# Kernel optimization log

Hardware: AMD Instinct MI355X
Metric: run time of the kernel (lower is better)

The kernel has to match this reference:

```python
import jax, jax.numpy as jnp
import numpy as np

H = 16      # num_heads
D = 64      # head_dim
SCALE = (2 * D) ** -0.5


def setup_inputs() -> dict:
    key = jax.random.key(0)
    k1, k2, k3, k4, k5 = jax.random.split(key, 5)
    tokens = jax.random.normal(k1, (4, 2048, 1024), dtype=jnp.float32)
    sen = jax.random.normal(k2, (4, 1, 1024), dtype=jnp.float32)
    W1 = jax.random.normal(k3, (1024, 3072), dtype=jnp.float32) * (1024 ** -0.5)
    W2 = jax.random.normal(k4, (1024, 2048), dtype=jnp.float32) * (1024 ** -0.5)
    mask = jax.random.randint(k5, (4, 2048), 0, 2, dtype=jnp.int32)
    return {"tokens": tokens, "sen": sen, "W1": W1, "W2": W2, "mask": mask}


def _split_heads(t):
    # [b, n, h*d] -> [b, h, n, d]
    b, n, _ = t.shape
    return t.reshape(b, n, H, D).transpose(0, 2, 1, 3)


def reference(tokens, sen, W1, W2, mask):
    b, n, _ = tokens.shape
    # token-stream qkv: [b, n, 3*h*d]
    q1, k1, v1 = (_split_heads(t) for t in jnp.split(tokens @ W1, 3, axis=-1))
    # sentence-stream qk: sen has seq len 1 -> [b, h, 1, d]
    q2, k2 = (_split_heads(t) for t in jnp.split(sen @ W2, 2, axis=-1))
    # dual-source scores: [b,h,n,n] + broadcast [b,h,1,1]
    dots = SCALE * (jnp.einsum('bhnd,bhmd->bhnm', q1, k1)
                    + jnp.einsum('bhnd,bhmd->bhnm', q2, k2))
    m = mask[:, None, None, :].astype(dots.dtype)
    dots = dots - 10000.0 * (1.0 - m)
    attn = jax.nn.softmax(dots, axis=-1)
    out = jnp.einsum('bhnm,bhmd->bhnd', attn, v1)
    return out.transpose(0, 2, 1, 3).reshape(b, n, H * D)
```

## Files before the change

### kernel.cpp

```cpp
#include <hip/hip_runtime.h>
#include <cstdint>


typedef __bf16 bf16x8 __attribute__((ext_vector_type(8)));
typedef __bf16 bf16x4 __attribute__((ext_vector_type(4)));
typedef float  f32x4  __attribute__((ext_vector_type(4)));
typedef float  f32x16 __attribute__((ext_vector_type(16)));
typedef unsigned int u32x4 __attribute__((ext_vector_type(4)));

#define MFMA16(a,b,c) __builtin_amdgcn_mfma_f32_16x16x32_bf16(a,b,c,0,0,0)
#define MFMA32(a,b,c) __builtin_amdgcn_mfma_f32_32x32x16_bf16(a,b,c,0,0,0)

static __device__ __forceinline__ float exp2_raw(float x) {
    float r; asm("v_exp_f32 %0, %1" : "=v"(r) : "v"(x)); return r;
}
static __device__ __forceinline__ uint32_t pkbf16(float a, float b) {
    uint32_t r; asm("v_cvt_pk_bf16_f32 %0, %1, %2" : "=v"(r) : "v"(a), "v"(b)); return r;
}
static __device__ __forceinline__ void lds_fence() {
    asm volatile("s_waitcnt lgkmcnt(0)" ::: "memory");
    __builtin_amdgcn_sched_barrier(0);
}
static __device__ __forceinline__ f32x16 zero16() {
    f32x16 z;
#pragma unroll
    for (int i = 0; i < 16; ++i) z[i] = 0.f;
    return z;
}
static __device__ __forceinline__ bf16x8 zero8() {
    return __builtin_bit_cast(bf16x8, (u32x4){0u, 0u, 0u, 0u});
}

#define GLLDS(src, dst)                                                        \
    __builtin_amdgcn_global_load_lds(                                          \
        (const __attribute__((address_space(1))) void*)(src),                  \
        (__attribute__((address_space(3))) void*)(dst), 16, 0, 0)

static constexpr float QSCALE = 0.12751879523486166f;

__global__ __launch_bounds__(256) void k_cvt_tok(const float* __restrict__ in,
                                                 __bf16* __restrict__ out) {
    int i = (blockIdx.x * 256 + threadIdx.x) * 4;
    float4 v = *(const float4*)&in[i];
    bf16x4 o = {(__bf16)v.x, (__bf16)v.y, (__bf16)v.z, (__bf16)v.w};
    *(bf16x4*)&out[i] = o;
}

__global__ __launch_bounds__(256) void k_w1t(const float* __restrict__ W1,
                                             __bf16* __restrict__ W1T) {
    __shared__ float t[32][33];
    int bx = blockIdx.x % 96, by = blockIdx.x / 96;
    int r0 = by * 32, c0 = bx * 32;
    int tr = threadIdx.x >> 3, tc = (threadIdx.x & 7) * 4;
    float4 v = *(const float4*)&W1[(size_t)(r0 + tr) * 3072 + c0 + tc];
    t[tr][tc + 0] = v.x; t[tr][tc + 1] = v.y; t[tr][tc + 2] = v.z; t[tr][tc + 3] = v.w;
    __syncthreads();
    bf16x4 o = {(__bf16)t[tc + 0][tr], (__bf16)t[tc + 1][tr],
                (__bf16)t[tc + 2][tr], (__bf16)t[tc + 3][tr]};
    *(bf16x4*)&W1T[(size_t)(c0 + tr) * 1024 + r0 + tc] = o;
}

__global__ __launch_bounds__(256) void k_mask(const int* __restrict__ m,
                                              __bf16* __restrict__ fl,
                                              __bf16* __restrict__ flp) {
    int i = blockIdx.x * 256 + threadIdx.x;
    fl[i] = (__bf16)(float)m[i];
    int s6 = i & 63;
    int kp = ((s6 >> 2) & 1) * 32 + ((s6 >> 4) & 3) * 8 + ((s6 >> 3) & 1) * 4 + (s6 & 3);
    flp[i] = (__bf16)(float)m[(i & ~63) | kp];
}

__global__ __launch_bounds__(256) void k_gemm_qkv(const __bf16* __restrict__ A,
                                                  const __bf16* __restrict__ BT,
                                                  const __bf16* __restrict__ FLAG,
                                                  __bf16* __restrict__ Q,
                                                  __bf16* __restrict__ K,
                                                  __bf16* __restrict__ VT) {
    __shared__ __align__(16) char gsm[32768];
    const int tid = threadIdx.x;
    const int bid = blockIdx.x;
    const int sw = (bid & 7) * 192 + (bid >> 3);
    const int tm = sw / 24, tn = sw % 24;
    const int m0 = tm * 128, n0 = tn * 128;
    const int l = tid & 63, wv = tid >> 6;
    const int l15 = l & 15, l4 = l >> 4;
    const int wr = wv >> 1, wc = wv & 1;

    const char* Ab = (const char*)A;
    const char* Bb = (const char*)BT;
    const size_t aoff = (size_t)(m0 + wv * 32 + (l >> 2)) * 2048 + (l & 3) * 16;
    const size_t boff = (size_t)(n0 + wv * 32 + (l >> 2)) * 2048 + (l & 3) * 16;

    f32x4 acc[4][4];
#pragma unroll
    for (int i = 0; i < 4; ++i)
#pragma unroll
        for (int j = 0; j < 4; ++j) acc[i][j] = (f32x4){0.f, 0.f, 0.f, 0.f};

    auto STAGE = [&](int nb, int kt) {
        char* ab = gsm + nb * 16384 + wv * 2048;
        char* bb = ab + 8192;
#pragma unroll
        for (int i = 0; i < 2; ++i) {
            GLLDS(Ab + aoff + (size_t)i * 32768 + (size_t)kt * 64, ab + i * 1024);
            GLLDS(Bb + boff + (size_t)i * 32768 + (size_t)kt * 64, bb + i * 1024);
        }
    };
    STAGE(0, 0);

    for (int kt = 0; kt < 32; ++kt) {
        const int cur = kt & 1;
        __syncthreads();
        if (kt < 31) STAGE(cur ^ 1, kt + 1);
        const char* As = gsm + cur * 16384;
        const char* Bs = As + 8192;

        bf16x8 af[4], bb[4];
#pragma unroll
        for (int mi = 0; mi < 4; ++mi)
            af[mi] = *(const bf16x8*)(As + (wr * 64 + mi * 16 + l15) * 64 + l4 * 16);
#pragma unroll
        for (int ni = 0; ni < 4; ++ni)
            bb[ni] = *(const bf16x8*)(Bs + (wc * 64 + ni * 16 + l15) * 64 + l4 * 16);
#pragma unroll
        for (int mi = 0; mi < 4; ++mi)
#pragma unroll
            for (int ni = 0; ni < 4; ++ni)
                acc[mi][ni] = MFMA16(af[mi], bb[ni], acc[mi][ni]);
    }

#pragma unroll
    for (int mi = 0; mi < 4; ++mi) {
        const int rowb = m0 + wr * 64 + mi * 16 + l4 * 4;
        const int b = rowb >> 11, n = rowb & 2047;
#pragma unroll
        for (int ni = 0; ni < 4; ++ni) {
            const int col = n0 + wc * 64 + ni * 16 + l15;
            const int str = col >> 10, cc = col & 1023;
            const int h = cc >> 6, d = cc & 63;
            const int bh = b * 16 + h;
            if (str == 2) {
                const bf16x4 fv = *(const bf16x4*)&FLAG[b * 2048 + n];
                bf16x4 pv = {(__bf16)(acc[mi][ni][0] * (float)fv[0]),
                             (__bf16)(acc[mi][ni][1] * (float)fv[1]),
                             (__bf16)(acc[mi][ni][2] * (float)fv[2]),
                             (__bf16)(acc[mi][ni][3] * (float)fv[3])};
                const int k6 = n & 63;
                const int nsl = (n & ~63) | (((k6 >> 3) & 3) << 4) |
                                (((k6 >> 2) & 1) << 3) | ((k6 >> 5) << 2);
                *(bf16x4*)&VT[((size_t)bh * 64 + d) * 2048 + nsl] = pv;
            } else if (str == 0) {
#pragma unroll
                for (int r = 0; r < 4; ++r)
                    Q[((size_t)bh * 2048 + n + r) * 64 + d] = (__bf16)(acc[mi][ni][r] * QSCALE);
            } else {
#pragma unroll
                for (int r = 0; r < 4; ++r)
                    K[((size_t)bh * 2048 + n + r) * 64 + d] = (__bf16)acc[mi][ni][r];
            }
        }
    }
}

__global__ __launch_bounds__(256, 2) void k_attn(const __bf16* __restrict__ Q,
                                                 const __bf16* __restrict__ K,
                                                 const __bf16* __restrict__ VT,
                                                 const __bf16* __restrict__ FLAGP,
                                                 float* __restrict__ out) {
    __shared__ __align__(16) char smem[33280];
    const int tid = threadIdx.x;
    const int bid = blockIdx.x;
    const int swz = (bid & 7) * 64 + (bid >> 3);
    const int bh = swz >> 3, qt = swz & 7;
    const int b = bh >> 4, h = bh & 15;
    const int wv = tid >> 6, l = tid & 63, l31 = l & 31, hi = l >> 5;

    const char* Kg = (const char*)K + (size_t)bh * 2048 * 128;
    const char* Vg = (const char*)VT + (size_t)bh * 64 * 4096;
    const __bf16* Fg = FLAGP + b * 2048;

    const __bf16* qp = Q + ((size_t)bh * 2048 + qt * 256 + wv * 64 + l31) * 64;
    bf16x8 qf0[4], qf1[4];
#pragma unroll
    for (int m = 0; m < 4; ++m) {
        qf0[m] = *(const bf16x8*)(qp + m * 16 + hi * 8);
        qf1[m] = *(const bf16x8*)(qp + 32 * 64 + m * 16 + hi * 8);
    }

    f32x16 o00 = zero16(), o01 = zero16(), o10 = zero16(), o11 = zero16();
    f32x16 fa0 = zero16(), fa1 = zero16();
    float mr0 = -1e30f, mr1 = -1e30f;

    auto STAGE = [&](int nb, int t) {
        char* base = smem + nb * 16384;
#pragma unroll
        for (int i = 0; i < 2; ++i) {
            const int blk = wv + i * 4;
            const int mc = blk >> 1, rb = blk & 1;
            const int row = rb * 32 + (l >> 1);
            GLLDS(Kg + (size_t)(t * 64 + row) * 128 + mc * 32 + (l & 1) * 16,
                  base + blk * 1024);
            GLLDS(Vg + (size_t)row * 4096 + t * 128 + mc * 32 + (l & 1) * 16,
                  base + 8192 + blk * 1024);
        }
    };
    STAGE(0, 0);

    for (int t = 0; t < 32; ++t) {
        const int cur = t & 1;
        __syncthreads();
        if (t < 31) STAGE(cur ^ 1, t + 1);
        const char* Ks = smem + cur * 16384;
        const char* Vs = Ks + 8192;

        bf16x8 kf0[4], kf1[4];
#pragma unroll
        for (int m = 0; m < 4; ++m) {
            kf0[m] = *(const bf16x8*)(Ks + m * 2048 + l31 * 32 + hi * 16);
            kf1[m] = *(const bf16x8*)(Ks + m * 2048 + (32 + l31) * 32 + hi * 16);
        }

        f32x16 s0 = zero16(), s1 = zero16();
#pragma unroll
        for (int m = 0; m < 4; ++m) s0 = MFMA32(kf0[m], qf0[m], s0);
#pragma unroll
        for (int m = 0; m < 4; ++m) s1 = MFMA32(kf1[m], qf0[m], s1);
        {
            float mx = fmaxf(s0[0], s1[0]);
#pragma unroll
            for (int i = 1; i < 16; ++i) mx = fmaxf(mx, fmaxf(s0[i], s1[i]));
            mx = fmaxf(mx, __shfl_xor(mx, 32, 64));
            if (!__all(mx <= mr0 + 8.0f)) {
                float mn = fmaxf(mr0, mx);
                float al = exp2_raw(mr0 - mn);
                o00 *= al; o01 *= al; fa0 *= al; mr0 = mn;
            }
        }
        u32x4 pk0[4];
#pragma unroll
        for (int m = 0; m < 4; ++m) {
            pk0[m].x = pkbf16(exp2_raw(s0[4 * m] - mr0), exp2_raw(s0[4 * m + 1] - mr0));
            pk0[m].y = pkbf16(exp2_raw(s0[4 * m + 2] - mr0), exp2_raw(s0[4 * m + 3] - mr0));
            pk0[m].z = pkbf16(exp2_raw(s1[4 * m] - mr0), exp2_raw(s1[4 * m + 1] - mr0));
            pk0[m].w = pkbf16(exp2_raw(s1[4 * m + 2] - mr0), exp2_raw(s1[4 * m + 3] - mr0));
        }

        bf16x8 ff[4];
#pragma unroll
        for (int m = 0; m < 4; ++m) ff[m] = zero8();
        if (l31 == 0) {
#pragma unroll
            for (int m = 0; m < 4; ++m)
                ff[m] = *(const bf16x8*)(Fg + t * 64 + m * 16 + hi * 8);
        }

        s0 = zero16(); s1 = zero16();
#pragma unroll
        for (int m = 0; m < 4; ++m) s0 = MFMA32(kf0[m], qf1[m], s0);
#pragma unroll
        for (int m = 0; m < 4; ++m) s1 = MFMA32(kf1[m], qf1[m], s1);
        {
            float mx = fmaxf(s0[0], s1[0]);
#pragma unroll
            for (int i = 1; i < 16; ++i) mx = fmaxf(mx, fmaxf(s0[i], s1[i]));
            mx = fmaxf(mx, __shfl_xor(mx, 32, 64));
            if (!__all(mx <= mr1 + 8.0f)) {
                float mn = fmaxf(mr1, mx);
                float al = exp2_raw(mr1 - mn);
                o10 *= al; o11 *= al; fa1 *= al; mr1 = mn;
            }
        }
        u32x4 pk1[4];
#pragma unroll
        for (int m = 0; m < 4; ++m) {
            pk1[m].x = pkbf16(exp2_raw(s0[4 * m] - mr1), exp2_raw(s0[4 * m + 1] - mr1));
            pk1[m].y = pkbf16(exp2_raw(s0[4 * m + 2] - mr1), exp2_raw(s0[4 * m + 3] - mr1));
            pk1[m].z = pkbf16(exp2_raw(s1[4 * m] - mr1), exp2_raw(s1[4 * m + 1] - mr1));
            pk1[m].w = pkbf16(exp2_raw(s1[4 * m + 2] - mr1), exp2_raw(s1[4 * m + 3] - mr1));
        }

#pragma unroll
        for (int m = 0; m < 4; ++m) {
            bf16x8 vf0 = *(const bf16x8*)(Vs + m * 2048 + l31 * 32 + hi * 16);
            bf16x8 vf1 = *(const bf16x8*)(Vs + m * 2048 + (32 + l31) * 32 + hi * 16);
            bf16x8 p0 = __builtin_bit_cast(bf16x8, pk0[m]);
            bf16x8 p1 = __builtin_bit_cast(bf16x8, pk1[m]);
            o00 = MFMA32(vf0, p0, o00);
            o01 = MFMA32(vf1, p0, o01);
            o10 = MFMA32(vf0, p1, o10);
            o11 = MFMA32(vf1, p1, o11);
            fa0 = MFMA32(ff[m], p0, fa0);
            fa1 = MFMA32(ff[m], p1, fa1);
        }
    }

    __syncthreads();
    float* osm = (float*)smem + wv * 2080;
    const size_t obase = ((size_t)b * 2048 + qt * 256 + wv * 64) * 1024 + h * 64 + l;
    {
        const float inv = 1.0f / __shfl(fa0[0], l31, 64);
#pragma unroll
        for (int r = 0; r < 16; ++r) {
            const int d = (r & 3) + 8 * (r >> 2) + 4 * hi;
            osm[l31 * 65 + d] = o00[r] * inv;
            osm[l31 * 65 + d + 32] = o01[r] * inv;
        }
        lds_fence();
#pragma unroll
        for (int qi = 0; qi < 32; ++qi)
            out[obase + (size_t)qi * 1024] = osm[qi * 65 + l];
        lds_fence();
    }
    {
        const float inv = 1.0f / __shfl(fa1[0], l31, 64);
#pragma unroll
        for (int r = 0; r < 16; ++r) {
            const int d = (r & 3) + 8 * (r >> 2) + 4 * hi;
            osm[l31 * 65 + d] = o10[r] * inv;
            osm[l31 * 65 + d + 32] = o11[r] * inv;
        }
        lds_fence();
#pragma unroll
        for (int qi = 0; qi < 32; ++qi)
            out[obase + (size_t)(32 + qi) * 1024] = osm[qi * 65 + l];
    }
}

extern "C" void kernel_launch(void* const* d_in, const int* in_sizes, int n_in,
                              void* d_out, int out_size, void* d_ws, size_t ws_size,
                              hipStream_t stream) {
    const float* tokens = (const float*)d_in[0];
    const float* W1 = (const float*)d_in[2];
    const int* mask = (const int*)d_in[4];
    float* out = (float*)d_out;

    char* w = (char*)d_ws;
    __bf16* tokbf = (__bf16*)(w + 0);
    __bf16* w1t   = (__bf16*)(w + 16777216);
    __bf16* qarr  = (__bf16*)(w + 23068672);
    __bf16* karr  = (__bf16*)(w + 39845888);
    __bf16* vtar  = (__bf16*)(w + 56623104);
    __bf16* flagb = (__bf16*)(w + 73400320);
    __bf16* flagp = (__bf16*)(w + 73416704);

    k_cvt_tok<<<8192, 256, 0, stream>>>(tokens, tokbf);
    k_w1t<<<3072, 256, 0, stream>>>(W1, w1t);
    k_mask<<<32, 256, 0, stream>>>(mask, flagb, flagp);
    k_gemm_qkv<<<1536, 256, 0, stream>>>(tokbf, w1t, flagb, qarr, karr, vtar);
    k_attn<<<512, 256, 0, stream>>>(qarr, karr, vtar, flagp, out);
}
```

Measured before the change: 264.8 us.

## Halve attention query tile per wave, double grid, stage Q/K GEMM epilogue through LDS

The attention kernel now gives each wave 32 query rows instead of 64, so the grid doubles to 1024 blocks and the launch bound rises to 4 blocks per SIMD. That cuts register pressure and raises occupancy, but K/V tiles are now reused across fewer queries, which doubles K/V traffic. s_setprio wraps the MFMA phases to favour matrix issue. Separately, the Q/K epilogue of the QKV GEMM stages bf16 results in LDS and writes them as contiguous 16-byte rows instead of scattered 2-byte stores.

```diff
diff --git a/kernel.cpp b/kernel.cpp
--- a/kernel.cpp
+++ b/kernel.cpp
@@ -76,7 +76,7 @@
                                                   __bf16* __restrict__ Q,
                                                   __bf16* __restrict__ K,
                                                   __bf16* __restrict__ VT) {
-    __shared__ __align__(16) char gsm[32768];
+    __shared__ __align__(16) char gsm[34816];
     const int tid = threadIdx.x;
     const int bid = blockIdx.x;
     const int sw = (bid & 7) * 192 + (bid >> 3);
@@ -129,18 +129,43 @@
                 acc[mi][ni] = MFMA16(af[mi], bb[ni], acc[mi][ni]);
     }
 
-#pragma unroll
-    for (int mi = 0; mi < 4; ++mi) {
-        const int rowb = m0 + wr * 64 + mi * 16 + l4 * 4;
-        const int b = rowb >> 11, n = rowb & 2047;
-#pragma unroll
-        for (int ni = 0; ni < 4; ++ni) {
-            const int col = n0 + wc * 64 + ni * 16 + l15;
-            const int str = col >> 10, cc = col & 1023;
-            const int h = cc >> 6, d = cc & 63;
-            const int bh = b * 16 + h;
-            if (str == 2) {
-                const bf16x4 fv = *(const bf16x4*)&FLAG[b * 2048 + n];
+    __syncthreads();
+
+    if (tn < 16) {
+        const float scl = (tn < 8) ? QSCALE : 1.0f;
+        char* csm = gsm;
+#pragma unroll
+        for (int mi = 0; mi < 4; ++mi) {
+            const int row = wr * 64 + mi * 16 + l4 * 4;
+#pragma unroll
+            for (int ni = 0; ni < 4; ++ni) {
+                const int col = wc * 64 + ni * 16 + l15;
+#pragma unroll
+                for (int r = 0; r < 4; ++r)
+                    *(__bf16*)(csm + (row + r) * 272 + col * 2) =
+                        (__bf16)(acc[mi][ni][r] * scl);
+            }
+        }
+        __syncthreads();
+        const int row = tid >> 1, hh = tid & 1;
+        const int rowg = m0 + row;
+        const int b = rowg >> 11, n = rowg & 2047;
+        const int h = ((n0 & 1023) >> 6) + hh;
+        __bf16* dst = ((tn < 8) ? Q : K) + ((size_t)(b * 16 + h) * 2048 + n) * 64;
+#pragma unroll
+        for (int j = 0; j < 8; ++j)
+            *(uint4*)(dst + j * 8) = *(const uint4*)(csm + row * 272 + hh * 128 + j * 16);
+    } else {
+#pragma unroll
+        for (int mi = 0; mi < 4; ++mi) {
+            const int rowb = m0 + wr * 64 + mi * 16 + l4 * 4;
+            const int b = rowb >> 11, n = rowb & 2047;
+            const bf16x4 fv = *(const bf16x4*)&FLAG[b * 2048 + n];
+#pragma unroll
+            for (int ni = 0; ni < 4; ++ni) {
+                const int col = n0 + wc * 64 + ni * 16 + l15;
+                const int cc = col & 1023;
+                const int h = cc >> 6, d = cc & 63;
                 bf16x4 pv = {(__bf16)(acc[mi][ni][0] * (float)fv[0]),
                              (__bf16)(acc[mi][ni][1] * (float)fv[1]),
                              (__bf16)(acc[mi][ni][2] * (float)fv[2]),
@@ -148,21 +173,13 @@
                 const int k6 = n & 63;
                 const int nsl = (n & ~63) | (((k6 >> 3) & 3) << 4) |
                                 (((k6 >> 2) & 1) << 3) | ((k6 >> 5) << 2);
-                *(bf16x4*)&VT[((size_t)bh * 64 + d) * 2048 + nsl] = pv;
-            } else if (str == 0) {
-#pragma unroll
-                for (int r = 0; r < 4; ++r)
-                    Q[((size_t)bh * 2048 + n + r) * 64 + d] = (__bf16)(acc[mi][ni][r] * QSCALE);
-            } else {
-#pragma unroll
-                for (int r = 0; r < 4; ++r)
-                    K[((size_t)bh * 2048 + n + r) * 64 + d] = (__bf16)acc[mi][ni][r];
+                *(bf16x4*)&VT[((size_t)(b * 16 + h) * 64 + d) * 2048 + nsl] = pv;
             }
         }
     }
 }
 
-__global__ __launch_bounds__(256, 2) void k_attn(const __bf16* __restrict__ Q,
+__global__ __launch_bounds__(256, 4) void k_attn(const __bf16* __restrict__ Q,
                                                  const __bf16* __restrict__ K,
                                                  const __bf16* __restrict__ VT,
                                                  const __bf16* __restrict__ FLAGP,
@@ -170,8 +187,8 @@
     __shared__ __align__(16) char smem[33280];
     const int tid = threadIdx.x;
     const int bid = blockIdx.x;
-    const int swz = (bid & 7) * 64 + (bid >> 3);
-    const int bh = swz >> 3, qt = swz & 7;
+    const int swz = (bid & 7) * 128 + (bid >> 3);
+    const int bh = swz >> 4, qt = swz & 15;
     const int b = bh >> 4, h = bh & 15;
     const int wv = tid >> 6, l = tid & 63, l31 = l & 31, hi = l >> 5;
 
@@ -179,17 +196,13 @@
     const char* Vg = (const char*)VT + (size_t)bh * 64 * 4096;
     const __bf16* Fg = FLAGP + b * 2048;
 
-    const __bf16* qp = Q + ((size_t)bh * 2048 + qt * 256 + wv * 64 + l31) * 64;
-    bf16x8 qf0[4], qf1[4];
-#pragma unroll
-    for (int m = 0; m < 4; ++m) {
-        qf0[m] = *(const bf16x8*)(qp + m * 16 + hi * 8);
-        qf1[m] = *(const bf16x8*)(qp + 32 * 64 + m * 16 + hi * 8);
-    }
-
-    f32x16 o00 = zero16(), o01 = zero16(), o10 = zero16(), o11 = zero16();
-    f32x16 fa0 = zero16(), fa1 = zero16();
-    float mr0 = -1e30f, mr1 = -1e30f;
+    const __bf16* qp = Q + ((size_t)bh * 2048 + qt * 128 + wv * 32 + l31) * 64;
+    bf16x8 qf[4];
+#pragma unroll
+    for (int m = 0; m < 4; ++m) qf[m] = *(const bf16x8*)(qp + m * 16 + hi * 8);
+
+    f32x16 o0 = zero16(), o1 = zero16(), fa = zero16();
+    float mr = -1e30f;
 
     auto STAGE = [&](int nb, int t) {
         char* base = smem + nb * 16384;
@@ -221,28 +234,31 @@
         }
 
         f32x16 s0 = zero16(), s1 = zero16();
-#pragma unroll
-        for (int m = 0; m < 4; ++m) s0 = MFMA32(kf0[m], qf0[m], s0);
-#pragma unroll
-        for (int m = 0; m < 4; ++m) s1 = MFMA32(kf1[m], qf0[m], s1);
+        __builtin_amdgcn_s_setprio(1);
+#pragma unroll
+        for (int m = 0; m < 4; ++m) s0 = MFMA32(kf0[m], qf[m], s0);
+#pragma unroll
+        for (int m = 0; m < 4; ++m) s1 = MFMA32(kf1[m], qf[m], s1);
+        __builtin_amdgcn_s_setprio(0);
+
         {
             float mx = fmaxf(s0[0], s1[0]);
 #pragma unroll
             for (int i = 1; i < 16; ++i) mx = fmaxf(mx, fmaxf(s0[i], s1[i]));
             mx = fmaxf(mx, __shfl_xor(mx, 32, 64));
-            if (!__all(mx <= mr0 + 8.0f)) {
-                float mn = fmaxf(mr0, mx);
-                float al = exp2_raw(mr0 - mn);
-                o00 *= al; o01 *= al; fa0 *= al; mr0 = mn;
+            if (!__all(mx <= mr + 8.0f)) {
+                float mn = fmaxf(mr, mx);
+                float al = exp2_raw(mr - mn);
+                o0 *= al; o1 *= al; fa *= al; mr = mn;
             }
         }
-        u32x4 pk0[4];
+        u32x4 pk[4];
 #pragma unroll
         for (int m = 0; m < 4; ++m) {
-            pk0[m].x = pkbf16(exp2_raw(s0[4 * m] - mr0), exp2_raw(s0[4 * m + 1] - mr0));
-            pk0[m].y = pkbf16(exp2_raw(s0[4 * m + 2] - mr0), exp2_raw(s0[4 * m + 3] - mr0));
-            pk0[m].z = pkbf16(exp2_raw(s1[4 * m] - mr0), exp2_raw(s1[4 * m + 1] - mr0));
-            pk0[m].w = pkbf16(exp2_raw(s1[4 * m + 2] - mr0), exp2_raw(s1[4 * m + 3] - mr0));
+            pk[m].x = pkbf16(exp2_raw(s0[4 * m] - mr), exp2_raw(s0[4 * m + 1] - mr));
+            pk[m].y = pkbf16(exp2_raw(s0[4 * m + 2] - mr), exp2_raw(s0[4 * m + 3] - mr));
+            pk[m].z = pkbf16(exp2_raw(s1[4 * m] - mr), exp2_raw(s1[4 * m + 1] - mr));
+            pk[m].w = pkbf16(exp2_raw(s1[4 * m + 2] - mr), exp2_raw(s1[4 * m + 3] - mr));
         }
 
         bf16x8 ff[4];
@@ -254,76 +270,33 @@
                 ff[m] = *(const bf16x8*)(Fg + t * 64 + m * 16 + hi * 8);
         }
 
-        s0 = zero16(); s1 = zero16();
-#pragma unroll
-        for (int m = 0; m < 4; ++m) s0 = MFMA32(kf0[m], qf1[m], s0);
-#pragma unroll
-        for (int m = 0; m < 4; ++m) s1 = MFMA32(kf1[m], qf1[m], s1);
-        {
-            float mx = fmaxf(s0[0], s1[0]);
-#pragma unroll
-            for (int i = 1; i < 16; ++i) mx = fmaxf(mx, fmaxf(s0[i], s1[i]));
-            mx = fmaxf(mx, __shfl_xor(mx, 32, 64));
-            if (!__all(mx <= mr1 + 8.0f)) {
-                float mn = fmaxf(mr1, mx);
-                float al = exp2_raw(mr1 - mn);
-                o10 *= al; o11 *= al; fa1 *= al; mr1 = mn;
-            }
-        }
-        u32x4 pk1[4];
-#pragma unroll
-        for (int m = 0; m < 4; ++m) {
-            pk1[m].x = pkbf16(exp2_raw(s0[4 * m] - mr1), exp2_raw(s0[4 * m + 1] - mr1));
-            pk1[m].y = pkbf16(exp2_raw(s0[4 * m + 2] - mr1), exp2_raw(s0[4 * m + 3] - mr1));
-            pk1[m].z = pkbf16(exp2_raw(s1[4 * m] - mr1), exp2_raw(s1[4 * m + 1] - mr1));
-            pk1[m].w = pkbf16(exp2_raw(s1[4 * m + 2] - mr1), exp2_raw(s1[4 * m + 3] - mr1));
-        }
-
+        __builtin_amdgcn_s_setprio(1);
 #pragma unroll
         for (int m = 0; m < 4; ++m) {
             bf16x8 vf0 = *(const bf16x8*)(Vs + m * 2048 + l31 * 32 + hi * 16);
             bf16x8 vf1 = *(const bf16x8*)(Vs + m * 2048 + (32 + l31) * 32 + hi * 16);
-            bf16x8 p0 = __builtin_bit_cast(bf16x8, pk0[m]);
-            bf16x8 p1 = __builtin_bit_cast(bf16x8, pk1[m]);
-            o00 = MFMA32(vf0, p0, o00);
-            o01 = MFMA32(vf1, p0, o01);
-            o10 = MFMA32(vf0, p1, o10);
-            o11 = MFMA32(vf1, p1, o11);
-            fa0 = MFMA32(ff[m], p0, fa0);
-            fa1 = MFMA32(ff[m], p1, fa1);
-        }
+            bf16x8 p = __builtin_bit_cast(bf16x8, pk[m]);
+            o0 = MFMA32(vf0, p, o0);
+            o1 = MFMA32(vf1, p, o1);
+            fa = MFMA32(ff[m], p, fa);
+        }
+        __builtin_amdgcn_s_setprio(0);
     }
 
     __syncthreads();
     float* osm = (float*)smem + wv * 2080;
-    const size_t obase = ((size_t)b * 2048 + qt * 256 + wv * 64) * 1024 + h * 64 + l;
-    {
-        const float inv = 1.0f / __shfl(fa0[0], l31, 64);
-#pragma unroll
-        for (int r = 0; r < 16; ++r) {
-            const int d = (r & 3) + 8 * (r >> 2) + 4 * hi;
-            osm[l31 * 65 + d] = o00[r] * inv;
-            osm[l31 * 65 + d + 32] = o01[r] * inv;
-        }
-        lds_fence();
-#pragma unroll
-        for (int qi = 0; qi < 32; ++qi)
-            out[obase + (size_t)qi * 1024] = osm[qi * 65 + l];
-        lds_fence();
+    const size_t obase = ((size_t)b * 2048 + qt * 128 + wv * 32) * 1024 + h * 64 + l;
+    const float inv = 1.0f / __shfl(fa[0], l31, 64);
+#pragma unroll
+    for (int r = 0; r < 16; ++r) {
+        const int d = (r & 3) + 8 * (r >> 2) + 4 * hi;
+        osm[l31 * 65 + d] = o0[r] * inv;
+        osm[l31 * 65 + d + 32] = o1[r] * inv;
     }
-    {
-        const float inv = 1.0f / __shfl(fa1[0], l31, 64);
-#pragma unroll
-        for (int r = 0; r < 16; ++r) {
-            const int d = (r & 3) + 8 * (r >> 2) + 4 * hi;
-            osm[l31 * 65 + d] = o10[r] * inv;
-            osm[l31 * 65 + d + 32] = o11[r] * inv;
-        }
-        lds_fence();
-#pragma unroll
-        for (int qi = 0; qi < 32; ++qi)
-            out[obase + (size_t)(32 + qi) * 1024] = osm[qi * 65 + l];
-    }
+    lds_fence();
+#pragma unroll
+    for (int qi = 0; qi < 32; ++qi)
+        out[obase + (size_t)qi * 1024] = osm[qi * 65 + l];
 }
 
 extern "C" void kernel_launch(void* const* d_in, const int* in_sizes, int n_in,
@@ -347,5 +320,5 @@
     k_w1t<<<3072, 256, 0, stream>>>(W1, w1t);
     k_mask<<<32, 256, 0, stream>>>(mask, flagb, flagp);
     k_gemm_qkv<<<1536, 256, 0, stream>>>(tokbf, w1t, flagb, qarr, karr, vtar);
-    k_attn<<<512, 256, 0, stream>>>(qarr, karr, vtar, flagp, out);
-}
+    k_attn<<<1024, 256, 0, stream>>>(qarr, karr, vtar, flagp, out);
+}
```

After: 280.8 us. +6.1%, slower.
